# Kernel optimization log

Measured on AMD Instinct MI355X. Metric: run time of the kernel, lower is better.

Reference implementation:

```python
import jax, jax.numpy as jnp
import numpy as np

NUM_USER = 100000
NUM_ITEM = 50000
DIM_E = 128
DIM_FEAT = 256
BATCH = 1024
NUM_NEG = 127
TEMP = 2.0
LR_LAMBDA = 0.5
NUM_SAMPLE = 0.5


def _l2norm(x, eps=1e-12):
    n = jnp.linalg.norm(x, axis=1, keepdims=True)
    return x / jnp.maximum(n, eps)


def setup_inputs() -> dict:
    key = jax.random.key(0)
    ks = jax.random.split(key, 9)
    flat = BATCH * (1 + NUM_NEG)
    user_tensor = jax.random.randint(ks[0], (BATCH, 1 + NUM_NEG), 0, NUM_USER, dtype=jnp.int64 if jax.config.jax_enable_x64 else jnp.int32)
    item_tensor = jax.random.randint(ks[1], (BATCH, 1 + NUM_NEG), NUM_USER, NUM_USER + NUM_ITEM, dtype=user_tensor.dtype)
    rand_index = jax.random.randint(ks[2], (int(flat * NUM_SAMPLE),), 0, flat, dtype=user_tensor.dtype)
    id_embedding = jax.random.normal(ks[3], (NUM_USER + NUM_ITEM, DIM_E), jnp.float32) * 0.02
    v_feat = jax.random.normal(ks[4], (NUM_ITEM, DIM_FEAT), jnp.float32)
    W1 = jax.random.normal(ks[5], (DIM_FEAT, 256), jnp.float32) * (1.0 / np.sqrt(DIM_FEAT))
    b1 = jax.random.normal(ks[6], (256,), jnp.float32) * 0.01
    W2 = jax.random.normal(ks[7], (256, DIM_E), jnp.float32) * (1.0 / 16.0)
    b2 = jax.random.normal(ks[8], (DIM_E,), jnp.float32) * 0.01
    return {"user_tensor": user_tensor, "item_tensor": item_tensor, "rand_index": rand_index,
            "id_embedding": id_embedding, "v_feat": v_feat, "W1": W1, "b1": b1, "W2": W2, "b2": b2}


def _contrastive(anchor, all_t):
    # exp(<a,b>/T) grouped into [B, 1+num_neg]; pos is column 0
    score = jnp.exp(jnp.sum(anchor * all_t, axis=1) / TEMP).reshape(-1, 1 + NUM_NEG)
    pos = score[:, 0]
    tot = jnp.sum(score, axis=1)
    return jnp.mean(-jnp.log(pos / tot))


def reference(user_tensor, item_tensor, rand_index, id_embedding, v_feat, W1, b1, W2, b2):
    # encoder: normalize content feats, 2-layer MLP
    feature = _l2norm(v_feat)
    feature = jax.nn.leaky_relu(feature @ W1 + b1)  # slope 0.01, matches torch default
    feature = feature @ W2 + b2                      # [num_item, dim_E]

    pos_flat = jnp.repeat(item_tensor[:, 0:1], 1 + NUM_NEG, axis=1).reshape(-1)
    u_flat = user_tensor.reshape(-1)
    i_flat = item_tensor.reshape(-1)

    all_item_feat = feature[i_flat - NUM_USER]          # [flat, dim_E]
    user_emb = id_embedding[u_flat]
    pos_emb = id_embedding[pos_flat]
    all_item_emb = id_embedding[i_flat]

    head_feat = _l2norm(all_item_feat)
    head_embed = _l2norm(pos_emb)

    # replace a random half of the item embeddings with content features
    all_item_input = all_item_emb.at[rand_index].set(all_item_feat[rand_index])

    c1 = _contrastive(head_embed, head_feat)
    c2 = _contrastive(user_emb, all_item_input)

    reg_loss = (jnp.mean(jnp.sqrt(jnp.sum(user_emb ** 2, axis=1))) +
                jnp.mean(jnp.sqrt(jnp.sum(all_item_emb ** 2, axis=1)))) / 2

    # graph_generator is None -> graph contrastive loss is 0
    total = c1 * LR_LAMBDA + c2 * (1.0 - LR_LAMBDA)
    return total, reg_loss
```

## Files before the change

### kernel.cpp

```cpp
#include <hip/hip_runtime.h>
#include <math.h>

#define NUSER 100000
#define NITEM 50000
#define NID   (NUSER + NITEM)
#define DIM_E 128
#define DIM_F 256
#define BATCH 1024
#define NCOL 128
#define FLAT (BATCH * NCOL)
#define NT   ((NITEM + 31) / 32)

typedef __attribute__((ext_vector_type(8))) short bf16x8;
typedef __attribute__((ext_vector_type(4))) short bf16x4;
typedef __attribute__((ext_vector_type(4))) float f32x4;

__device__ __forceinline__ float dot4(float4 a, float4 b) {
    return a.x * b.x + a.y * b.y + a.z * b.z + a.w * b.w;
}

__device__ __forceinline__ short f2bf(float x) {
    unsigned u = __float_as_uint(x);
    unsigned r = (u + 0x7FFFu + ((u >> 16) & 1u)) >> 16;
    return (short)r;
}

__device__ __forceinline__ float bf2f(short s) {
    return __uint_as_float(((unsigned)(unsigned short)s) << 16);
}

__global__ __launch_bounds__(256) void prep0_kernel(const float* __restrict__ W1,
                                                    const float* __restrict__ W2,
                                                    short* __restrict__ w1t,
                                                    short* __restrict__ w2t,
                                                    int* __restrict__ flags) {
    int i = blockIdx.x * 256 + threadIdx.x;
    if (i < FLAT) flags[i] = 0;
    if (i < 256 * 256) {
        int n = i >> 8, k = i & 255;
        w1t[i] = f2bf(W1[(size_t)k * 256 + n]);
    } else if (i < 256 * 256 + 128 * 256) {
        int j = i - 256 * 256;
        int n = j >> 8, k = j & 255;
        w2t[j] = f2bf(W2[(size_t)k * 128 + n]);
    }
}

__global__ __launch_bounds__(256) void stream_kernel(const float* __restrict__ vfeat,
                                                     short* __restrict__ vfeatn,
                                                     const float* __restrict__ idemb,
                                                     short* __restrict__ idemb_bf,
                                                     float* __restrict__ norms,
                                                     const int* __restrict__ ridx,
                                                     int nridx,
                                                     int* __restrict__ flags) {
    const int t = threadIdx.x;
    if (blockIdx.x < 768) {
        const int wv = blockIdx.x * 4 + (t >> 6);
        const int l = t & 63;
        for (int row = wv; row < NITEM; row += 3072) {
            float4 v = *(const float4*)(vfeat + (size_t)row * DIM_F + l * 4);
            float s = dot4(v, v);
#pragma unroll
            for (int off = 32; off >= 1; off >>= 1) s += __shfl_xor(s, off);
            float inv = 1.f / fmaxf(sqrtf(s), 1e-12f);
            bf16x4 p;
            p[0] = f2bf(v.x * inv); p[1] = f2bf(v.y * inv);
            p[2] = f2bf(v.z * inv); p[3] = f2bf(v.w * inv);
            *(bf16x4*)(vfeatn + (size_t)row * DIM_F + l * 4) = p;
        }
    } else {
        const int blk = blockIdx.x - 768;
        if (blk < 128) {
            for (int i = blk * 256 + t; i < nridx; i += 128 * 256) flags[ridx[i]] = 1;
        }
        const int sub = t & 31;
        int row = blk * 8 + (t >> 5);
        for (; row < NID; row += 1280 * 8) {
            float4 v = *(const float4*)(idemb + (size_t)row * DIM_E + sub * 4);
            float s = dot4(v, v);
#pragma unroll
            for (int off = 16; off >= 1; off >>= 1) s += __shfl_xor(s, off);
            bf16x4 p;
            p[0] = f2bf(v.x); p[1] = f2bf(v.y); p[2] = f2bf(v.z); p[3] = f2bf(v.w);
            *(bf16x4*)(idemb_bf + (size_t)row * DIM_E + sub * 4) = p;
            if (sub == 0) norms[row] = sqrtf(s);
        }
    }
}

__global__ __launch_bounds__(512, 2) void mlp_mfma_kernel(const short* __restrict__ vfeatn,
                                                          const short* __restrict__ w1t,
                                                          const float* __restrict__ b1,
                                                          const short* __restrict__ w2t,
                                                          const float* __restrict__ b2,
                                                          short* __restrict__ featout) {
    __shared__ __align__(16) short As[32 * 256];
    __shared__ __align__(16) short Hs[32 * 256];
    const int t = threadIdx.x;
    const int w = t >> 6;
    const int l = t & 63;
    const int fr = l & 15;
    const int kg = l >> 4;
    const int srow = t >> 4;
    const int q = t & 15;
    const int sw = (srow & 7) << 3;

    bf16x8 B1f[8][2];
    bf16x8 B2f[8];
#pragma unroll
    for (int kc = 0; kc < 8; ++kc) {
#pragma unroll
        for (int ct = 0; ct < 2; ++ct)
            B1f[kc][ct] = *(const bf16x8*)(w1t + (size_t)(w * 32 + ct * 16 + fr) * 256 + kc * 32 + kg * 8);
        B2f[kc] = *(const bf16x8*)(w2t + (size_t)(w * 16 + fr) * 256 + kc * 32 + kg * 8);
    }
    float b1v[2];
    b1v[0] = b1[w * 32 + fr];
    b1v[1] = b1[w * 32 + 16 + fr];
    const float b2v = b2[w * 16 + fr];

    int tile = blockIdx.x;
    {
        bf16x8 r0 = {0,0,0,0,0,0,0,0}, r1 = {0,0,0,0,0,0,0,0};
        int gr = tile * 32 + srow;
        if (gr < NITEM) {
            const bf16x8* s = (const bf16x8*)(vfeatn + (size_t)gr * DIM_F + q * 16);
            r0 = s[0]; r1 = s[1];
        }
        *(bf16x8*)(&As[srow * 256 + ((q * 16) ^ sw)]) = r0;
        *(bf16x8*)(&As[srow * 256 + ((q * 16 + 8) ^ sw)]) = r1;
    }
    __syncthreads();

    while (tile < NT) {
        const int tnext = tile + 256;
        bf16x8 n0 = {0,0,0,0,0,0,0,0}, n1 = {0,0,0,0,0,0,0,0};
        if (tnext < NT) {
            int gr = tnext * 32 + srow;
            if (gr < NITEM) {
                const bf16x8* s = (const bf16x8*)(vfeatn + (size_t)gr * DIM_F + q * 16);
                n0 = s[0]; n1 = s[1];
            }
        }

        {
            f32x4 acc1[2][2];
#pragma unroll
            for (int rt = 0; rt < 2; ++rt)
#pragma unroll
                for (int ct = 0; ct < 2; ++ct) acc1[rt][ct] = (f32x4){0.f, 0.f, 0.f, 0.f};
#pragma unroll
            for (int kc = 0; kc < 8; ++kc) {
                const int kb = kc * 32 + kg * 8;
                bf16x8 af[2];
#pragma unroll
                for (int rt = 0; rt < 2; ++rt) {
                    int row = rt * 16 + fr;
                    af[rt] = *(const bf16x8*)(&As[row * 256 + (kb ^ ((row & 7) << 3))]);
                }
#pragma unroll
                for (int ct = 0; ct < 2; ++ct)
#pragma unroll
                    for (int rt = 0; rt < 2; ++rt)
                        acc1[rt][ct] = __builtin_amdgcn_mfma_f32_16x16x32_bf16(af[rt], B1f[kc][ct], acc1[rt][ct], 0, 0, 0);
            }
#pragma unroll
            for (int rt = 0; rt < 2; ++rt)
#pragma unroll
                for (int ct = 0; ct < 2; ++ct) {
                    int colH = w * 32 + ct * 16 + fr;
#pragma unroll
                    for (int r = 0; r < 4; ++r) {
                        float h = acc1[rt][ct][r] + b1v[ct];
                        h = h > 0.f ? h : 0.01f * h;
                        int row = rt * 16 + kg * 4 + r;
                        Hs[row * 256 + (colH ^ ((row & 7) << 3))] = f2bf(h);
                    }
                }
        }
        __syncthreads();

        {
            f32x4 acc2[2];
            acc2[0] = (f32x4){0.f, 0.f, 0.f, 0.f};
            acc2[1] = (f32x4){0.f, 0.f, 0.f, 0.f};
#pragma unroll
            for (int kc = 0; kc < 8; ++kc) {
                const int kb = kc * 32 + kg * 8;
#pragma unroll
                for (int rt = 0; rt < 2; ++rt) {
                    int row = rt * 16 + fr;
                    bf16x8 hf = *(const bf16x8*)(&Hs[row * 256 + (kb ^ ((row & 7) << 3))]);
                    acc2[rt] = __builtin_amdgcn_mfma_f32_16x16x32_bf16(hf, B2f[kc], acc2[rt], 0, 0, 0);
                }
            }
            const int col = w * 16 + fr;
#pragma unroll
            for (int rt = 0; rt < 2; ++rt)
#pragma unroll
                for (int r = 0; r < 4; ++r) {
                    int row = tile * 32 + rt * 16 + kg * 4 + r;
                    if (row < NITEM) featout[(size_t)row * DIM_E + col] = f2bf(acc2[rt][r] + b2v);
                }
        }

        if (tnext < NT) {
            *(bf16x8*)(&As[srow * 256 + ((q * 16) ^ sw)]) = n0;
            *(bf16x8*)(&As[srow * 256 + ((q * 16 + 8) ^ sw)]) = n1;
        }
        __syncthreads();
        tile = tnext;
    }
}

__global__ __launch_bounds__(128) void contrast_kernel(const int* __restrict__ user,
                                                       const int* __restrict__ item,
                                                       const int* __restrict__ flags,
                                                       const short* __restrict__ idemb_bf,
                                                       const float* __restrict__ norms,
                                                       const short* __restrict__ feat,
                                                       float* __restrict__ rowpart) {
    __shared__ float pe[128];
    __shared__ float s1s[64], s2s[64], rs[64];
    __shared__ float dpos[2];
    const int row = blockIdx.x >> 1;
    const int part = blockIdx.x & 1;
    const int t = threadIdx.x;

    if (t < 32) {
        int p = item[(size_t)row * NCOL];
        float inv = 1.f / fmaxf(norms[p], 1e-12f);
        bf16x4 v = *(const bf16x4*)(idemb_bf + (size_t)p * DIM_E + t * 4);
        pe[t * 4 + 0] = bf2f(v[0]) * inv;
        pe[t * 4 + 1] = bf2f(v[1]) * inv;
        pe[t * 4 + 2] = bf2f(v[2]) * inv;
        pe[t * 4 + 3] = bf2f(v[3]) * inv;
    }
    __syncthreads();

    const int el = t >> 1;
    const int e = part * 64 + el;
    const int h = t & 1;
    const size_t j = (size_t)row * NCOL + e;
    const int u = user[j];
    const int it = item[j];
    const int fl = flags[j];
    const short* up = idemb_bf + (size_t)u * DIM_E + h * 64;
    const short* ip = idemb_bf + (size_t)it * DIM_E + h * 64;
    const short* fp = feat + (size_t)(it - NUSER) * DIM_E + h * 64;

    bf16x8 ub[8], fb[8], xb[8];
#pragma unroll
    for (int i = 0; i < 8; ++i) { ub[i] = ((const bf16x8*)up)[i]; fb[i] = ((const bf16x8*)fp)[i]; }
    if (fl) {
#pragma unroll
        for (int i = 0; i < 8; ++i) xb[i] = fb[i];
    } else {
#pragma unroll
        for (int i = 0; i < 8; ++i) xb[i] = ((const bf16x8*)ip)[i];
    }
    float nu = norms[u];
    float ni = norms[it];

    float sf = 0.f, dpf = 0.f, dux = 0.f;
#pragma unroll
    for (int i = 0; i < 8; ++i) {
        float4 p0 = *(const float4*)(&pe[h * 64 + i * 8]);
        float4 p1 = *(const float4*)(&pe[h * 64 + i * 8 + 4]);
        float pk[8] = {p0.x, p0.y, p0.z, p0.w, p1.x, p1.y, p1.z, p1.w};
#pragma unroll
        for (int k = 0; k < 8; ++k) {
            float fv = bf2f(fb[i][k]);
            float uv = bf2f(ub[i][k]);
            float xv = bf2f(xb[i][k]);
            sf += fv * fv;
            dpf += pk[k] * fv;
            dux += uv * xv;
        }
    }
    sf += __shfl_xor(sf, 1);
    dpf += __shfl_xor(dpf, 1);
    dux += __shfl_xor(dux, 1);

    if (h == 0) {
        float fnorm = fmaxf(sqrtf(sf), 1e-12f);
        float d1 = dpf / fnorm * 0.5f;
        float d2 = dux * 0.5f;
        s1s[el] = expf(d1);
        s2s[el] = expf(d2);
        rs[el] = nu + ni;
        if (e == 0) { dpos[0] = d1; dpos[1] = d2; }
    }
    __syncthreads();

    if (t < 32) {
        float a1 = s1s[t] + s1s[t + 32];
        float a2 = s2s[t] + s2s[t + 32];
        float a3 = rs[t] + rs[t + 32];
#pragma unroll
        for (int off = 16; off >= 1; off >>= 1) {
            a1 += __shfl_xor(a1, off);
            a2 += __shfl_xor(a2, off);
            a3 += __shfl_xor(a3, off);
        }
        if (t == 0) {
            float* dst = rowpart + (size_t)blockIdx.x * 6;
            dst[0] = a1;
            dst[1] = a2;
            dst[2] = a3;
            if (part == 0) { dst[3] = dpos[0]; dst[4] = dpos[1]; }
        }
    }
}

__global__ __launch_bounds__(256) void finalize_kernel(const float* __restrict__ rowpart,
                                                       float* __restrict__ out) {
    float c1 = 0.f, c2 = 0.f, rg = 0.f;
    for (int r = threadIdx.x; r < BATCH; r += 256) {
        const float* p0 = rowpart + (size_t)(r * 2) * 6;
        const float* p1 = rowpart + (size_t)(r * 2 + 1) * 6;
        float A1 = p0[0] + p1[0];
        float A2 = p0[1] + p1[1];
        c1 += logf(A1) - p0[3];
        c2 += logf(A2) - p0[4];
        rg += p0[2] + p1[2];
    }
#pragma unroll
    for (int off = 32; off >= 1; off >>= 1) {
        c1 += __shfl_xor(c1, off);
        c2 += __shfl_xor(c2, off);
        rg += __shfl_xor(rg, off);
    }
    __shared__ float buf[4][3];
    int wid = threadIdx.x >> 6, lane = threadIdx.x & 63;
    if (lane == 0) { buf[wid][0] = c1; buf[wid][1] = c2; buf[wid][2] = rg; }
    __syncthreads();
    if (threadIdx.x == 0) {
        float C1 = buf[0][0] + buf[1][0] + buf[2][0] + buf[3][0];
        float C2 = buf[0][1] + buf[1][1] + buf[2][1] + buf[3][1];
        float R  = buf[0][2] + buf[1][2] + buf[2][2] + buf[3][2];
        out[0] = 0.5f * (C1 / (float)BATCH) + 0.5f * (C2 / (float)BATCH);
        out[1] = 0.5f * (R / (float)FLAT);
    }
}

extern "C" void kernel_launch(void* const* d_in, const int* in_sizes, int n_in,
                              void* d_out, int out_size, void* d_ws, size_t ws_size,
                              hipStream_t stream) {
    const int* user = (const int*)d_in[0];
    const int* item = (const int*)d_in[1];
    const int* ridx = (const int*)d_in[2];
    const float* idemb = (const float*)d_in[3];
    const float* vfeat = (const float*)d_in[4];
    const float* W1 = (const float*)d_in[5];
    const float* b1 = (const float*)d_in[6];
    const float* W2 = (const float*)d_in[7];
    const float* b2 = (const float*)d_in[8];
    float* out = (float*)d_out;

    char* ws = (char*)d_ws;
    short* feat_bf  = (short*)(ws);
    short* idemb_bf = (short*)(ws + 12800000);
    short* vfeatn   = (short*)(ws + 51200000);
    float* norms    = (float*)(ws + 76800000);
    int*   flags    = (int*)  (ws + 77400000);
    float* rowpart  = (float*)(ws + 77924288);
    short* w1t      = (short*)(ws + 77973440);
    short* w2t      = (short*)(ws + 78104512);

    const int nridx = in_sizes[2];

    prep0_kernel<<<dim3(512), dim3(256), 0, stream>>>(W1, W2, w1t, w2t, flags);
    stream_kernel<<<dim3(2048), dim3(256), 0, stream>>>(vfeat, vfeatn, idemb, idemb_bf,
                                                        norms, ridx, nridx, flags);
    mlp_mfma_kernel<<<dim3(256), dim3(512), 0, stream>>>(vfeatn, w1t, b1, w2t, b2, feat_bf);
    contrast_kernel<<<dim3(2 * BATCH), dim3(128), 0, stream>>>(user, item, flags,
                                                               idemb_bf, norms, feat_bf, rowpart);
    finalize_kernel<<<dim3(1), dim3(256), 0, stream>>>(rowpart, out);
}
```

Baseline: 83.55 us.

## Defer row normalization into MLP epilogue and recompute norms in contrast kernel

The fused stream kernel, which did per-row reductions to L2-normalize v_feat and precompute id-embedding norms, becomes a flat grid-stride fp32-to-bf16 conversion. The v_feat normalization moves into the MLP: per-row inverse norms are computed from the staged bf16 tile and applied to the first GEMM's accumulator before the bias, using linearity. The contrast kernel now recomputes user and item norms from bf16 data and always loads the item embedding, which removes the norms buffer and its gathers. In exchange there is some extra ALU work and loads in the contrast and MLP kernels, and norms computed from bf16 values are slightly less precise.

```diff
diff --git a/kernel.cpp b/kernel.cpp
--- a/kernel.cpp
+++ b/kernel.cpp
@@ -46,50 +46,35 @@
     }
 }
 
-__global__ __launch_bounds__(256) void stream_kernel(const float* __restrict__ vfeat,
-                                                     short* __restrict__ vfeatn,
-                                                     const float* __restrict__ idemb,
-                                                     short* __restrict__ idemb_bf,
-                                                     float* __restrict__ norms,
-                                                     const int* __restrict__ ridx,
-                                                     int nridx,
-                                                     int* __restrict__ flags) {
-    const int t = threadIdx.x;
-    if (blockIdx.x < 768) {
-        const int wv = blockIdx.x * 4 + (t >> 6);
-        const int l = t & 63;
-        for (int row = wv; row < NITEM; row += 3072) {
-            float4 v = *(const float4*)(vfeat + (size_t)row * DIM_F + l * 4);
-            float s = dot4(v, v);
-#pragma unroll
-            for (int off = 32; off >= 1; off >>= 1) s += __shfl_xor(s, off);
-            float inv = 1.f / fmaxf(sqrtf(s), 1e-12f);
-            bf16x4 p;
-            p[0] = f2bf(v.x * inv); p[1] = f2bf(v.y * inv);
-            p[2] = f2bf(v.z * inv); p[3] = f2bf(v.w * inv);
-            *(bf16x4*)(vfeatn + (size_t)row * DIM_F + l * 4) = p;
-        }
-    } else {
-        const int blk = blockIdx.x - 768;
-        if (blk < 128) {
-            for (int i = blk * 256 + t; i < nridx; i += 128 * 256) flags[ridx[i]] = 1;
-        }
-        const int sub = t & 31;
-        int row = blk * 8 + (t >> 5);
-        for (; row < NID; row += 1280 * 8) {
-            float4 v = *(const float4*)(idemb + (size_t)row * DIM_E + sub * 4);
-            float s = dot4(v, v);
-#pragma unroll
-            for (int off = 16; off >= 1; off >>= 1) s += __shfl_xor(s, off);
-            bf16x4 p;
-            p[0] = f2bf(v.x); p[1] = f2bf(v.y); p[2] = f2bf(v.z); p[3] = f2bf(v.w);
-            *(bf16x4*)(idemb_bf + (size_t)row * DIM_E + sub * 4) = p;
-            if (sub == 0) norms[row] = sqrtf(s);
-        }
-    }
-}
-
-__global__ __launch_bounds__(512, 2) void mlp_mfma_kernel(const short* __restrict__ vfeatn,
+__global__ __launch_bounds__(256) void convert_kernel(const float* __restrict__ vfeat,
+                                                      short* __restrict__ vfeat_bf,
+                                                      const float* __restrict__ idemb,
+                                                      short* __restrict__ idemb_bf,
+                                                      const int* __restrict__ ridx,
+                                                      int nridx,
+                                                      int* __restrict__ flags) {
+    const int tid = blockIdx.x * 256 + threadIdx.x;
+    if (blockIdx.x < 128) {
+        for (int i = tid; i < nridx; i += 128 * 256) flags[ridx[i]] = 1;
+    }
+    const int NV8 = NITEM * DIM_F / 8;
+    const int NT8 = NV8 + NID * DIM_E / 8;
+    const int stride = gridDim.x * 256;
+    for (int i = tid; i < NT8; i += stride) {
+        const float* src;
+        short* dst;
+        if (i < NV8) { src = vfeat + (size_t)i * 8;           dst = vfeat_bf + (size_t)i * 8; }
+        else         { size_t j = (size_t)(i - NV8) * 8;      src = idemb + j; dst = idemb_bf + j; }
+        float4 a = *(const float4*)src;
+        float4 b = *(const float4*)(src + 4);
+        bf16x8 p;
+        p[0] = f2bf(a.x); p[1] = f2bf(a.y); p[2] = f2bf(a.z); p[3] = f2bf(a.w);
+        p[4] = f2bf(b.x); p[5] = f2bf(b.y); p[6] = f2bf(b.z); p[7] = f2bf(b.w);
+        *(bf16x8*)dst = p;
+    }
+}
+
+__global__ __launch_bounds__(512, 2) void mlp_mfma_kernel(const short* __restrict__ vfeat_bf,
                                                           const short* __restrict__ w1t,
                                                           const float* __restrict__ b1,
                                                           const short* __restrict__ w2t,
@@ -97,6 +82,7 @@
                                                           short* __restrict__ featout) {
     __shared__ __align__(16) short As[32 * 256];
     __shared__ __align__(16) short Hs[32 * 256];
+    __shared__ float invn[32];
     const int t = threadIdx.x;
     const int w = t >> 6;
     const int l = t & 63;
@@ -120,16 +106,31 @@
     b1v[1] = b1[w * 32 + 16 + fr];
     const float b2v = b2[w * 16 + fr];
 
+#define STAGE_AND_NORM(R0, R1)                                                  \
+    {                                                                           \
+        *(bf16x8*)(&As[srow * 256 + ((q * 16) ^ sw)]) = (R0);                   \
+        *(bf16x8*)(&As[srow * 256 + ((q * 16 + 8) ^ sw)]) = (R1);               \
+        float s_ = 0.f;                                                         \
+        _Pragma("unroll")                                                       \
+        for (int k_ = 0; k_ < 8; ++k_) { float x_ = bf2f((R0)[k_]); s_ = fmaf(x_, x_, s_); } \
+        _Pragma("unroll")                                                       \
+        for (int k_ = 0; k_ < 8; ++k_) { float x_ = bf2f((R1)[k_]); s_ = fmaf(x_, x_, s_); } \
+        s_ += __shfl_xor(s_, 1);                                                \
+        s_ += __shfl_xor(s_, 2);                                                \
+        s_ += __shfl_xor(s_, 4);                                                \
+        s_ += __shfl_xor(s_, 8);                                                \
+        if (q == 0) invn[srow] = 1.f / fmaxf(sqrtf(s_), 1e-12f);                \
+    }
+
     int tile = blockIdx.x;
     {
         bf16x8 r0 = {0,0,0,0,0,0,0,0}, r1 = {0,0,0,0,0,0,0,0};
         int gr = tile * 32 + srow;
         if (gr < NITEM) {
-            const bf16x8* s = (const bf16x8*)(vfeatn + (size_t)gr * DIM_F + q * 16);
+            const bf16x8* s = (const bf16x8*)(vfeat_bf + (size_t)gr * DIM_F + q * 16);
             r0 = s[0]; r1 = s[1];
         }
-        *(bf16x8*)(&As[srow * 256 + ((q * 16) ^ sw)]) = r0;
-        *(bf16x8*)(&As[srow * 256 + ((q * 16 + 8) ^ sw)]) = r1;
+        STAGE_AND_NORM(r0, r1)
     }
     __syncthreads();
 
@@ -139,7 +140,7 @@
         if (tnext < NT) {
             int gr = tnext * 32 + srow;
             if (gr < NITEM) {
-                const bf16x8* s = (const bf16x8*)(vfeatn + (size_t)gr * DIM_F + q * 16);
+                const bf16x8* s = (const bf16x8*)(vfeat_bf + (size_t)gr * DIM_F + q * 16);
                 n0 = s[0]; n1 = s[1];
             }
         }
@@ -172,9 +173,9 @@
                     int colH = w * 32 + ct * 16 + fr;
 #pragma unroll
                     for (int r = 0; r < 4; ++r) {
-                        float h = acc1[rt][ct][r] + b1v[ct];
+                        int row = rt * 16 + kg * 4 + r;
+                        float h = invn[row] * acc1[rt][ct][r] + b1v[ct];
                         h = h > 0.f ? h : 0.01f * h;
-                        int row = rt * 16 + kg * 4 + r;
                         Hs[row * 256 + (colH ^ ((row & 7) << 3))] = f2bf(h);
                     }
                 }
@@ -206,19 +207,18 @@
         }
 
         if (tnext < NT) {
-            *(bf16x8*)(&As[srow * 256 + ((q * 16) ^ sw)]) = n0;
-            *(bf16x8*)(&As[srow * 256 + ((q * 16 + 8) ^ sw)]) = n1;
+            STAGE_AND_NORM(n0, n1)
         }
         __syncthreads();
         tile = tnext;
     }
+#undef STAGE_AND_NORM
 }
 
 __global__ __launch_bounds__(128) void contrast_kernel(const int* __restrict__ user,
                                                        const int* __restrict__ item,
                                                        const int* __restrict__ flags,
                                                        const short* __restrict__ idemb_bf,
-                                                       const float* __restrict__ norms,
                                                        const short* __restrict__ feat,
                                                        float* __restrict__ rowpart) {
     __shared__ float pe[128];
@@ -230,12 +230,16 @@
 
     if (t < 32) {
         int p = item[(size_t)row * NCOL];
-        float inv = 1.f / fmaxf(norms[p], 1e-12f);
         bf16x4 v = *(const bf16x4*)(idemb_bf + (size_t)p * DIM_E + t * 4);
-        pe[t * 4 + 0] = bf2f(v[0]) * inv;
-        pe[t * 4 + 1] = bf2f(v[1]) * inv;
-        pe[t * 4 + 2] = bf2f(v[2]) * inv;
-        pe[t * 4 + 3] = bf2f(v[3]) * inv;
+        float f0 = bf2f(v[0]), f1 = bf2f(v[1]), f2 = bf2f(v[2]), f3 = bf2f(v[3]);
+        float s = f0 * f0 + f1 * f1 + f2 * f2 + f3 * f3;
+#pragma unroll
+        for (int off = 16; off >= 1; off >>= 1) s += __shfl_xor(s, off);
+        float inv = 1.f / fmaxf(sqrtf(s), 1e-12f);
+        pe[t * 4 + 0] = f0 * inv;
+        pe[t * 4 + 1] = f1 * inv;
+        pe[t * 4 + 2] = f2 * inv;
+        pe[t * 4 + 3] = f3 * inv;
     }
     __syncthreads();
 
@@ -250,20 +254,15 @@
     const short* ip = idemb_bf + (size_t)it * DIM_E + h * 64;
     const short* fp = feat + (size_t)(it - NUSER) * DIM_E + h * 64;
 
-    bf16x8 ub[8], fb[8], xb[8];
-#pragma unroll
-    for (int i = 0; i < 8; ++i) { ub[i] = ((const bf16x8*)up)[i]; fb[i] = ((const bf16x8*)fp)[i]; }
-    if (fl) {
-#pragma unroll
-        for (int i = 0; i < 8; ++i) xb[i] = fb[i];
-    } else {
-#pragma unroll
-        for (int i = 0; i < 8; ++i) xb[i] = ((const bf16x8*)ip)[i];
-    }
-    float nu = norms[u];
-    float ni = norms[it];
-
-    float sf = 0.f, dpf = 0.f, dux = 0.f;
+    bf16x8 ub[8], ib[8], fb[8];
+#pragma unroll
+    for (int i = 0; i < 8; ++i) {
+        ub[i] = ((const bf16x8*)up)[i];
+        ib[i] = ((const bf16x8*)ip)[i];
+        fb[i] = ((const bf16x8*)fp)[i];
+    }
+
+    float su = 0.f, si = 0.f, sf = 0.f, dpf = 0.f, dux = 0.f;
 #pragma unroll
     for (int i = 0; i < 8; ++i) {
         float4 p0 = *(const float4*)(&pe[h * 64 + i * 8]);
@@ -273,12 +272,17 @@
         for (int k = 0; k < 8; ++k) {
             float fv = bf2f(fb[i][k]);
             float uv = bf2f(ub[i][k]);
-            float xv = bf2f(xb[i][k]);
-            sf += fv * fv;
-            dpf += pk[k] * fv;
-            dux += uv * xv;
-        }
-    }
+            float iv = bf2f(ib[i][k]);
+            float xv = fl ? fv : iv;
+            su = fmaf(uv, uv, su);
+            si = fmaf(iv, iv, si);
+            sf = fmaf(fv, fv, sf);
+            dpf = fmaf(pk[k], fv, dpf);
+            dux = fmaf(uv, xv, dux);
+        }
+    }
+    su += __shfl_xor(su, 1);
+    si += __shfl_xor(si, 1);
     sf += __shfl_xor(sf, 1);
     dpf += __shfl_xor(dpf, 1);
     dux += __shfl_xor(dux, 1);
@@ -289,7 +293,7 @@
         float d2 = dux * 0.5f;
         s1s[el] = expf(d1);
         s2s[el] = expf(d2);
-        rs[el] = nu + ni;
+        rs[el] = sqrtf(su) + sqrtf(si);
         if (e == 0) { dpos[0] = d1; dpos[1] = d2; }
     }
     __syncthreads();
@@ -362,20 +366,19 @@
     char* ws = (char*)d_ws;
     short* feat_bf  = (short*)(ws);
     short* idemb_bf = (short*)(ws + 12800000);
-    short* vfeatn   = (short*)(ws + 51200000);
-    float* norms    = (float*)(ws + 76800000);
-    int*   flags    = (int*)  (ws + 77400000);
-    float* rowpart  = (float*)(ws + 77924288);
-    short* w1t      = (short*)(ws + 77973440);
-    short* w2t      = (short*)(ws + 78104512);
+    short* vfeat_bf = (short*)(ws + 51200000);
+    int*   flags    = (int*)  (ws + 76800000);
+    float* rowpart  = (float*)(ws + 77324288);
+    short* w1t      = (short*)(ws + 77373440);
+    short* w2t      = (short*)(ws + 77504512);
 
     const int nridx = in_sizes[2];
 
     prep0_kernel<<<dim3(512), dim3(256), 0, stream>>>(W1, W2, w1t, w2t, flags);
-    stream_kernel<<<dim3(2048), dim3(256), 0, stream>>>(vfeat, vfeatn, idemb, idemb_bf,
-                                                        norms, ridx, nridx, flags);
-    mlp_mfma_kernel<<<dim3(256), dim3(512), 0, stream>>>(vfeatn, w1t, b1, w2t, b2, feat_bf);
+    convert_kernel<<<dim3(2048), dim3(256), 0, stream>>>(vfeat, vfeat_bf, idemb, idemb_bf,
+                                                         ridx, nridx, flags);
+    mlp_mfma_kernel<<<dim3(256), dim3(512), 0, stream>>>(vfeat_bf, w1t, b1, w2t, b2, feat_bf);
     contrast_kernel<<<dim3(2 * BATCH), dim3(128), 0, stream>>>(user, item, flags,
-                                                               idemb_bf, norms, feat_bf, rowpart);
+                                                               idemb_bf, feat_bf, rowpart);
     finalize_kernel<<<dim3(1), dim3(256), 0, stream>>>(rowpart, out);
 }
```

Measured after the change: 109.8 us. +31.4%, slower.

## Split fp32-to-bf16 conversion from norm computation and fold normalization into MLP

Applied to the files above, without the earlier changes.

Replaces the combined stream kernel with a flat, high-parallelism convert kernel that turns vfeat and id embeddings into bf16 using 4 independent loads per thread. A separate norms kernel then computes row norms from the bf16 copies, and the per-row inverse norm of vfeat is applied inside the MLP epilogue rather than pre-scaling the inputs. The aim is more memory-level parallelism in the dominant fp32 streaming pass. In exchange it adds a kernel launch and an extra read of the bf16 buffers, and the norms are computed from rounded values.

```diff
diff --git a/kernel.cpp b/kernel.cpp
--- a/kernel.cpp
+++ b/kernel.cpp
@@ -10,6 +10,9 @@
 #define NCOL 128
 #define FLAT (BATCH * NCOL)
 #define NT   ((NITEM + 31) / 32)
+#define NV8  (NITEM * DIM_F / 8)
+#define NT8  (NV8 + NID * DIM_E / 8)
+#define CONV_BLOCKS 3907
 
 typedef __attribute__((ext_vector_type(8))) short bf16x8;
 typedef __attribute__((ext_vector_type(4))) short bf16x4;
@@ -46,50 +49,80 @@
     }
 }
 
-__global__ __launch_bounds__(256) void stream_kernel(const float* __restrict__ vfeat,
-                                                     short* __restrict__ vfeatn,
-                                                     const float* __restrict__ idemb,
-                                                     short* __restrict__ idemb_bf,
-                                                     float* __restrict__ norms,
-                                                     const int* __restrict__ ridx,
-                                                     int nridx,
-                                                     int* __restrict__ flags) {
+__global__ __launch_bounds__(256) void convert_kernel(const float* __restrict__ vfeat,
+                                                      short* __restrict__ vfeat_bf,
+                                                      const float* __restrict__ idemb,
+                                                      short* __restrict__ idemb_bf,
+                                                      const int* __restrict__ ridx,
+                                                      int nridx,
+                                                      int* __restrict__ flags) {
+    const int tid = blockIdx.x * 256 + threadIdx.x;
+    if (blockIdx.x < 128) {
+        for (int i = tid; i < nridx; i += 128 * 256) flags[ridx[i]] = 1;
+    }
+    const int T = CONV_BLOCKS * 256;
+    float4 a[4], b[4];
+#pragma unroll
+    for (int k = 0; k < 4; ++k) {
+        int i = tid + k * T;
+        const float* src = (i < NV8) ? vfeat + (size_t)i * 8
+                                     : idemb + (size_t)(i - NV8) * 8;
+        if (i < NT8) {
+            a[k] = *(const float4*)src;
+            b[k] = *(const float4*)(src + 4);
+        } else {
+            a[k] = make_float4(0.f, 0.f, 0.f, 0.f);
+            b[k] = make_float4(0.f, 0.f, 0.f, 0.f);
+        }
+    }
+#pragma unroll
+    for (int k = 0; k < 4; ++k) {
+        int i = tid + k * T;
+        if (i < NT8) {
+            short* dst = (i < NV8) ? vfeat_bf + (size_t)i * 8
+                                   : idemb_bf + (size_t)(i - NV8) * 8;
+            bf16x8 p;
+            p[0] = f2bf(a[k].x); p[1] = f2bf(a[k].y); p[2] = f2bf(a[k].z); p[3] = f2bf(a[k].w);
+            p[4] = f2bf(b[k].x); p[5] = f2bf(b[k].y); p[6] = f2bf(b[k].z); p[7] = f2bf(b[k].w);
+            *(bf16x8*)dst = p;
+        }
+    }
+}
+
+__global__ __launch_bounds__(256) void norms_kernel(const short* __restrict__ vfeat_bf,
+                                                    const short* __restrict__ idemb_bf,
+                                                    float* __restrict__ invn_v,
+                                                    float* __restrict__ norms) {
     const int t = threadIdx.x;
-    if (blockIdx.x < 768) {
-        const int wv = blockIdx.x * 4 + (t >> 6);
-        const int l = t & 63;
-        for (int row = wv; row < NITEM; row += 3072) {
-            float4 v = *(const float4*)(vfeat + (size_t)row * DIM_F + l * 4);
-            float s = dot4(v, v);
-#pragma unroll
-            for (int off = 32; off >= 1; off >>= 1) s += __shfl_xor(s, off);
-            float inv = 1.f / fmaxf(sqrtf(s), 1e-12f);
-            bf16x4 p;
-            p[0] = f2bf(v.x * inv); p[1] = f2bf(v.y * inv);
-            p[2] = f2bf(v.z * inv); p[3] = f2bf(v.w * inv);
-            *(bf16x4*)(vfeatn + (size_t)row * DIM_F + l * 4) = p;
+    if (blockIdx.x < 512) {
+        const int grp = (blockIdx.x * 256 + t) >> 5;
+        const int sub = t & 31;
+        for (int row = grp; row < NITEM; row += 4096) {
+            bf16x8 v = *(const bf16x8*)(vfeat_bf + (size_t)row * DIM_F + sub * 8);
+            float s = 0.f;
+#pragma unroll
+            for (int k = 0; k < 8; ++k) { float x = bf2f(v[k]); s = fmaf(x, x, s); }
+#pragma unroll
+            for (int off = 16; off >= 1; off >>= 1) s += __shfl_xor(s, off);
+            if (sub == 0) invn_v[row] = 1.f / fmaxf(sqrtf(s), 1e-12f);
         }
     } else {
-        const int blk = blockIdx.x - 768;
-        if (blk < 128) {
-            for (int i = blk * 256 + t; i < nridx; i += 128 * 256) flags[ridx[i]] = 1;
-        }
-        const int sub = t & 31;
-        int row = blk * 8 + (t >> 5);
-        for (; row < NID; row += 1280 * 8) {
-            float4 v = *(const float4*)(idemb + (size_t)row * DIM_E + sub * 4);
-            float s = dot4(v, v);
-#pragma unroll
-            for (int off = 16; off >= 1; off >>= 1) s += __shfl_xor(s, off);
-            bf16x4 p;
-            p[0] = f2bf(v.x); p[1] = f2bf(v.y); p[2] = f2bf(v.z); p[3] = f2bf(v.w);
-            *(bf16x4*)(idemb_bf + (size_t)row * DIM_E + sub * 4) = p;
+        const int grp = ((blockIdx.x - 512) * 256 + t) >> 4;
+        const int sub = t & 15;
+        for (int row = grp; row < NID; row += 24576) {
+            bf16x8 v = *(const bf16x8*)(idemb_bf + (size_t)row * DIM_E + sub * 8);
+            float s = 0.f;
+#pragma unroll
+            for (int k = 0; k < 8; ++k) { float x = bf2f(v[k]); s = fmaf(x, x, s); }
+#pragma unroll
+            for (int off = 8; off >= 1; off >>= 1) s += __shfl_xor(s, off);
             if (sub == 0) norms[row] = sqrtf(s);
         }
     }
 }
 
-__global__ __launch_bounds__(512, 2) void mlp_mfma_kernel(const short* __restrict__ vfeatn,
+__global__ __launch_bounds__(512, 2) void mlp_mfma_kernel(const short* __restrict__ vfeat_bf,
+                                                          const float* __restrict__ invn_v,
                                                           const short* __restrict__ w1t,
                                                           const float* __restrict__ b1,
                                                           const short* __restrict__ w2t,
@@ -125,7 +158,7 @@
         bf16x8 r0 = {0,0,0,0,0,0,0,0}, r1 = {0,0,0,0,0,0,0,0};
         int gr = tile * 32 + srow;
         if (gr < NITEM) {
-            const bf16x8* s = (const bf16x8*)(vfeatn + (size_t)gr * DIM_F + q * 16);
+            const bf16x8* s = (const bf16x8*)(vfeat_bf + (size_t)gr * DIM_F + q * 16);
             r0 = s[0]; r1 = s[1];
         }
         *(bf16x8*)(&As[srow * 256 + ((q * 16) ^ sw)]) = r0;
@@ -139,10 +172,18 @@
         if (tnext < NT) {
             int gr = tnext * 32 + srow;
             if (gr < NITEM) {
-                const bf16x8* s = (const bf16x8*)(vfeatn + (size_t)gr * DIM_F + q * 16);
+                const bf16x8* s = (const bf16x8*)(vfeat_bf + (size_t)gr * DIM_F + q * 16);
                 n0 = s[0]; n1 = s[1];
             }
         }
+        float invr[2][4];
+#pragma unroll
+        for (int rt = 0; rt < 2; ++rt)
+#pragma unroll
+            for (int r = 0; r < 4; ++r) {
+                int gr = tile * 32 + rt * 16 + kg * 4 + r;
+                invr[rt][r] = (gr < NITEM) ? invn_v[gr] : 0.f;
+            }
 
         {
             f32x4 acc1[2][2];
@@ -172,9 +213,9 @@
                     int colH = w * 32 + ct * 16 + fr;
 #pragma unroll
                     for (int r = 0; r < 4; ++r) {
-                        float h = acc1[rt][ct][r] + b1v[ct];
+                        int row = rt * 16 + kg * 4 + r;
+                        float h = invr[rt][r] * acc1[rt][ct][r] + b1v[ct];
                         h = h > 0.f ? h : 0.01f * h;
-                        int row = rt * 16 + kg * 4 + r;
                         Hs[row * 256 + (colH ^ ((row & 7) << 3))] = f2bf(h);
                     }
                 }
@@ -274,9 +315,9 @@
             float fv = bf2f(fb[i][k]);
             float uv = bf2f(ub[i][k]);
             float xv = bf2f(xb[i][k]);
-            sf += fv * fv;
-            dpf += pk[k] * fv;
-            dux += uv * xv;
+            sf = fmaf(fv, fv, sf);
+            dpf = fmaf(pk[k], fv, dpf);
+            dux = fmaf(uv, xv, dux);
         }
     }
     sf += __shfl_xor(sf, 1);
@@ -362,19 +403,21 @@
     char* ws = (char*)d_ws;
     short* feat_bf  = (short*)(ws);
     short* idemb_bf = (short*)(ws + 12800000);
-    short* vfeatn   = (short*)(ws + 51200000);
+    short* vfeat_bf = (short*)(ws + 51200000);
     float* norms    = (float*)(ws + 76800000);
-    int*   flags    = (int*)  (ws + 77400000);
-    float* rowpart  = (float*)(ws + 77924288);
-    short* w1t      = (short*)(ws + 77973440);
-    short* w2t      = (short*)(ws + 78104512);
+    float* invn_v   = (float*)(ws + 77400000);
+    int*   flags    = (int*)  (ws + 77600000);
+    float* rowpart  = (float*)(ws + 78124288);
+    short* w1t      = (short*)(ws + 78173440);
+    short* w2t      = (short*)(ws + 78304512);
 
     const int nridx = in_sizes[2];
 
     prep0_kernel<<<dim3(512), dim3(256), 0, stream>>>(W1, W2, w1t, w2t, flags);
-    stream_kernel<<<dim3(2048), dim3(256), 0, stream>>>(vfeat, vfeatn, idemb, idemb_bf,
-                                                        norms, ridx, nridx, flags);
-    mlp_mfma_kernel<<<dim3(256), dim3(512), 0, stream>>>(vfeatn, w1t, b1, w2t, b2, feat_bf);
+    convert_kernel<<<dim3(CONV_BLOCKS), dim3(256), 0, stream>>>(vfeat, vfeat_bf, idemb, idemb_bf,
+                                                                ridx, nridx, flags);
+    norms_kernel<<<dim3(2048), dim3(256), 0, stream>>>(vfeat_bf, idemb_bf, invn_v, norms);
+    mlp_mfma_kernel<<<dim3(256), dim3(512), 0, stream>>>(vfeat_bf, invn_v, w1t, b1, w2t, b2, feat_bf);
     contrast_kernel<<<dim3(2 * BATCH), dim3(128), 0, stream>>>(user, item, flags,
                                                                idemb_bf, norms, feat_bf, rowpart);
     finalize_kernel<<<dim3(1), dim3(256), 0, stream>>>(rowpart, out);
```

Result: slower. 96.27 us (+15.2%).
